# Kernel optimization log

Measured on AMD Instinct MI355X. Metric: run time of the kernel, lower is better.

## Reference

```python
import jax, jax.numpy as jnp
import numpy as np

N, C, H, W = 16, 512, 32, 32
OC = C // 8  # shrink = 8


def setup_inputs() -> dict:
    key = jax.random.key(0)
    ks = jax.random.split(key, 8)
    s = lambda fan: 1.0 / np.sqrt(fan)
    return {
        "tensor": jax.random.normal(ks[0], (N, C, H, W), dtype=jnp.float32),
        "key_w": jax.random.normal(ks[1], (OC, C), dtype=jnp.float32) * s(C),
        "key_b": jax.random.normal(ks[2], (OC,), dtype=jnp.float32) * 0.01,
        "query_w": jax.random.normal(ks[3], (OC, C), dtype=jnp.float32) * s(C),
        "query_b": jax.random.normal(ks[4], (OC,), dtype=jnp.float32) * 0.01,
        "value_w": jax.random.normal(ks[5], (C, C), dtype=jnp.float32) * s(C),
        "value_b": jax.random.normal(ks[6], (C,), dtype=jnp.float32) * 0.01,
        "gamma": jax.random.normal(ks[7], (1,), dtype=jnp.float32),
    }


def reference(tensor, key_w, key_b, query_w, query_b, value_w, value_b, gamma):
    n, c, h, w = tensor.shape
    x = tensor.reshape(n, c, h * w)  # [n, c, hw]
    # 1x1 convs are per-position linear maps over channels
    k = jnp.einsum("oc,ncp->nop", key_w, x) + key_b[None, :, None]      # [n, oc, hw]
    q = jnp.einsum("oc,ncp->nop", query_w, x) + query_b[None, :, None]  # [n, oc, hw]
    v = jnp.einsum("oc,ncp->nop", value_w, x) + value_b[None, :, None]  # [n, c, hw]
    # unscaled attention: softmax over keys (last dim)
    scores = jnp.einsum("ncq,nck->nqk", q, k)  # [n, hw, hw]
    attn = jax.nn.softmax(scores, axis=2)
    o = jnp.einsum("nck,nqk->ncq", v, attn).reshape(n, c, h, w)
    return tensor + o * gamma[0]
```

## Files before the change

kernel.cpp:

```cpp
#include <hip/hip_runtime.h>
#include <hip/hip_bf16.h>

typedef __hip_bfloat16 bf16;
typedef __attribute__((ext_vector_type(8))) short bf16x8;
typedef __attribute__((ext_vector_type(4))) float f32x4;

#define NBATCH 16
#define CCH    512
#define PP     1024
#define OCH    64

__device__ __forceinline__ void gload16(const void* g, void* l) {
  __builtin_amdgcn_global_load_lds(
      (const __attribute__((address_space(1))) void*)g,
      (__attribute__((address_space(3))) void*)l, 16, 0, 0);
}
__device__ __forceinline__ float bf2f(bf16 v) { return __bfloat162float(v); }
__device__ __forceinline__ bf16  f2bf(float v) { return __float2bfloat16(v); }

__device__ __forceinline__ void barrier_vm0() {
  asm volatile("s_waitcnt vmcnt(0)" ::: "memory");
  __builtin_amdgcn_s_barrier();
  asm volatile("" ::: "memory");
}
__device__ __forceinline__ void barrier_lgkm0() {
  asm volatile("s_waitcnt lgkmcnt(0)" ::: "memory");
  __builtin_amdgcn_s_barrier();
  asm volatile("" ::: "memory");
}

__global__ void prep_kernel(const float* __restrict__ key_w, const float* __restrict__ key_b,
                            const float* __restrict__ query_w, const float* __restrict__ query_b,
                            const float* __restrict__ value_w, const float* __restrict__ value_b,
                            bf16* __restrict__ wqk_hi, bf16* __restrict__ wqk_lo,
                            bf16* __restrict__ wv, float* __restrict__ bias_qk,
                            float* __restrict__ bias_v) {
  const int t = blockIdx.x * blockDim.x + threadIdx.x;
  const int TOT_QK = 128 * 512;
  const int TOT_V  = 512 * 512;
  if (t < TOT_QK) {
    const int m = t >> 9, c = t & 511;
    const float v = (m < 64) ? query_w[m * 512 + c] : key_w[(m - 64) * 512 + c];
    const bf16 hi = f2bf(v);
    wqk_hi[t] = hi;
    wqk_lo[t] = f2bf(v - bf2f(hi));
  } else if (t < TOT_QK + TOT_V) {
    const int u = t - TOT_QK;
    wv[u] = f2bf(value_w[u]);
  } else if (t < TOT_QK + TOT_V + 128) {
    const int m = t - (TOT_QK + TOT_V);
    bias_qk[m] = (m < 64) ? query_b[m] : key_b[m - 64];
  } else if (t < TOT_QK + TOT_V + 128 + 512) {
    const int m = t - (TOT_QK + TOT_V + 128);
    bias_v[m] = value_b[m];
  }
}

__global__ __launch_bounds__(256) void gemm_qkv_kernel(
    const bf16* __restrict__ Whi, const bf16* __restrict__ Wlo,
    const bf16* __restrict__ Wv, const float* __restrict__ x,
    const float* __restrict__ biasqk, const float* __restrict__ biasv,
    bf16* __restrict__ qhi, bf16* __restrict__ qlo,
    bf16* __restrict__ khi, bf16* __restrict__ klo,
    bf16* __restrict__ Vout) {
  __shared__ __align__(16) char sm[65536];
  const int tid = threadIdx.x, l = tid & 63, w = tid >> 6;
  const int li = l & 15, g = l >> 4;
  const int lrow = l >> 3, lcol = (l & 7) * 8, wr = w >> 1, wc = w & 1;
  const int tp = tid >> 1;
  const int tch = (tid & 1) * 32;
  const f32x4 z = {0.f, 0.f, 0.f, 0.f};
  f32x4 acc[4][4];
#pragma unroll
  for (int i = 0; i < 4; ++i)
#pragma unroll
    for (int j = 0; j < 4; ++j) acc[i][j] = z;

  char* Xs  = sm + 32768;
  char* Bsh = sm + 32768;
  char* Bsl = sm + 49152;

  if (blockIdx.x < 128) {
    const int id = blockIdx.x;
    const int n0 = (id & 7) * 128, bn = id >> 3;
    const float* xb = x + (size_t)bn * CCH * PP;
    bf16* Ash = (bf16*)sm;
    bf16* Asl = (bf16*)(sm + 16384);

    for (int kt = 0; kt < CCH; kt += 64) {
#pragma unroll
      for (int it = 0; it < 4; ++it) {
        const int chunk = w * 4 + it;
        const int ar = chunk * 8 + lrow;
        gload16(Whi + (size_t)ar * CCH + kt + lcol, &Ash[chunk * 512]);
        gload16(Wlo + (size_t)ar * CCH + kt + lcol, &Asl[chunk * 512]);
      }
#pragma unroll
      for (int i = 0; i < 8; ++i) {
        const int s = i * 256 + w * 64 + l;
        const int row = s >> 5, col16 = s & 31;
        gload16(xb + (size_t)(kt + row) * PP + n0 + col16 * 4,
                Xs + (i * 256 + w * 64) * 16);
      }
      __syncthreads();

      float f[32];
#pragma unroll
      for (int k = 0; k < 32; ++k)
        f[k] = *(const float*)(Xs + (size_t)(tch + k) * 512 + tp * 4);
      barrier_lgkm0();
#pragma unroll
      for (int k2 = 0; k2 < 4; ++k2) {
        bf16x8 hv, lv;
#pragma unroll
        for (int j = 0; j < 8; ++j) {
          const float ff = f[k2 * 8 + j];
          const bf16 h = f2bf(ff);
          const bf16 lo_ = f2bf(ff - bf2f(h));
          short hs, ls;
          __builtin_memcpy(&hs, &h, 2);
          __builtin_memcpy(&ls, &lo_, 2);
          hv[j] = hs;
          lv[j] = ls;
        }
        const int chunk = (tch >> 3) + k2;
        const int pu = chunk ^ (tp & 7);
        *(bf16x8*)(Bsh + tp * 128 + pu * 16) = hv;
        *(bf16x8*)(Bsl + tp * 128 + pu * 16) = lv;
      }
      barrier_lgkm0();

#pragma unroll
      for (int kk = 0; kk < 2; ++kk) {
        bf16x8 ah[4], al[4], bh[4], bl[4];
        const int ko = kk * 32 + g * 8;
#pragma unroll
        for (int i = 0; i < 4; ++i) {
          const int r = (wr * 64 + i * 16 + li) * 64 + ko;
          ah[i] = *(const bf16x8*)&Ash[r];
          al[i] = *(const bf16x8*)&Asl[r];
        }
#pragma unroll
        for (int j = 0; j < 4; ++j) {
          const int row = wc * 64 + j * 16 + li;
          const int pu = (4 * kk + g) ^ (row & 7);
          bh[j] = *(const bf16x8*)(Bsh + row * 128 + pu * 16);
          bl[j] = *(const bf16x8*)(Bsl + row * 128 + pu * 16);
        }
#pragma unroll
        for (int i = 0; i < 4; ++i)
#pragma unroll
          for (int j = 0; j < 4; ++j) {
            acc[i][j] = __builtin_amdgcn_mfma_f32_16x16x32_bf16(ah[i], bh[j], acc[i][j], 0, 0, 0);
            acc[i][j] = __builtin_amdgcn_mfma_f32_16x16x32_bf16(ah[i], bl[j], acc[i][j], 0, 0, 0);
            acc[i][j] = __builtin_amdgcn_mfma_f32_16x16x32_bf16(al[i], bh[j], acc[i][j], 0, 0, 0);
          }
      }
      __syncthreads();
    }
    const size_t qoff = (size_t)bn * PP * OCH;
#pragma unroll
    for (int i = 0; i < 4; ++i)
#pragma unroll
      for (int j = 0; j < 4; ++j)
#pragma unroll
        for (int r = 0; r < 4; ++r) {
          const int m = wr * 64 + i * 16 + g * 4 + r;
          const int p = n0 + wc * 64 + j * 16 + li;
          const float v = acc[i][j][r] + biasqk[m];
          const bf16 hi = f2bf(v);
          const bf16 lo = f2bf(v - bf2f(hi));
          if (m < 64) {
            qhi[qoff + (size_t)p * OCH + m] = hi;
            qlo[qoff + (size_t)p * OCH + m] = lo;
          } else {
            khi[qoff + (size_t)p * OCH + (m - 64)] = hi;
            klo[qoff + (size_t)p * OCH + (m - 64)] = lo;
          }
        }
  } else {
    const int id = blockIdx.x - 128;
    const int n0 = (id & 7) * 128, m0 = ((id >> 3) & 3) * 128, bn = id >> 5;
    const float* xb = x + (size_t)bn * CCH * PP;
    bf16* As = (bf16*)sm;

    for (int kt = 0; kt < CCH; kt += 64) {
#pragma unroll
      for (int it = 0; it < 4; ++it) {
        const int chunk = w * 4 + it;
        gload16(Wv + (size_t)(m0 + chunk * 8 + lrow) * CCH + kt + lcol, &As[chunk * 512]);
      }
#pragma unroll
      for (int i = 0; i < 8; ++i) {
        const int s = i * 256 + w * 64 + l;
        const int row = s >> 5, col16 = s & 31;
        gload16(xb + (size_t)(kt + row) * PP + n0 + col16 * 4,
                Xs + (i * 256 + w * 64) * 16);
      }
      __syncthreads();

      float f[32];
#pragma unroll
      for (int k = 0; k < 32; ++k)
        f[k] = *(const float*)(Xs + (size_t)(tch + k) * 512 + tp * 4);
      barrier_lgkm0();
#pragma unroll
      for (int k2 = 0; k2 < 4; ++k2) {
        bf16x8 hv;
#pragma unroll
        for (int j = 0; j < 8; ++j) {
          const bf16 h = f2bf(f[k2 * 8 + j]);
          short hs;
          __builtin_memcpy(&hs, &h, 2);
          hv[j] = hs;
        }
        const int chunk = (tch >> 3) + k2;
        const int pu = chunk ^ (tp & 7);
        *(bf16x8*)(Bsh + tp * 128 + pu * 16) = hv;
      }
      barrier_lgkm0();

#pragma unroll
      for (int kk = 0; kk < 2; ++kk) {
        bf16x8 a[4], b[4];
        const int ko = kk * 32 + g * 8;
#pragma unroll
        for (int i = 0; i < 4; ++i) a[i] = *(const bf16x8*)&As[(wr * 64 + i * 16 + li) * 64 + ko];
#pragma unroll
        for (int j = 0; j < 4; ++j) {
          const int row = wc * 64 + j * 16 + li;
          const int pu = (4 * kk + g) ^ (row & 7);
          b[j] = *(const bf16x8*)(Bsh + row * 128 + pu * 16);
        }
#pragma unroll
        for (int i = 0; i < 4; ++i)
#pragma unroll
          for (int j = 0; j < 4; ++j)
            acc[i][j] = __builtin_amdgcn_mfma_f32_16x16x32_bf16(a[i], b[j], acc[i][j], 0, 0, 0);
      }
      __syncthreads();
    }
#pragma unroll
    for (int i = 0; i < 4; ++i)
#pragma unroll
      for (int j = 0; j < 4; ++j)
#pragma unroll
        for (int r = 0; r < 4; ++r) {
          const int m = m0 + wr * 64 + i * 16 + g * 4 + r;
          const int p = n0 + wc * 64 + j * 16 + li;
          Vout[(size_t)bn * CCH * PP + (size_t)m * PP + p] = f2bf(acc[i][j][r] + biasv[m]);
        }
  }
}

#define KT 32
#define NT 32

__global__ __launch_bounds__(512, 2) void fused_attn_kernel(
    const bf16* __restrict__ qhi, const bf16* __restrict__ qlo,
    const bf16* __restrict__ khi, const bf16* __restrict__ klo,
    const bf16* __restrict__ vbuf, const float* __restrict__ tensor,
    const float* __restrict__ gamma, float* __restrict__ out) {
  __shared__ __align__(16) char smem[102400];
  __shared__ float red[128];
  __shared__ float fq[64];
  const int tid = threadIdx.x, l = tid & 63, w = tid >> 6;

  const int d = blockIdx.x;
  const int idx = d >> 3;
  const int bn = (d & 7) * 2 + (idx >> 4);
  const int qt0 = (idx & 15) * 64;

  const size_t qkoff = (size_t)bn * PP * OCH;
  const size_t voff  = (size_t)bn * CCH * PP;
  char* Qh = smem;
  char* Ql = smem + 8192;
  char* Pb = smem + 98304;

  {
    const int s = (w << 6) | l;
    const int row = s >> 3, pu = s & 7, lu = pu ^ (row & 7);
    const size_t src = qkoff + (size_t)(qt0 + row) * OCH + lu * 8;
    gload16(qhi + src, Qh + w * 1024);
    gload16(qlo + src, Ql + w * 1024);
  }
  barrier_vm0();

  bf16x8 ah[2], al[2];
  {
    const int qrow = ((w & 3) << 4) + (l & 15);
#pragma unroll
    for (int h = 0; h < 2; ++h) {
      const int lu = (l >> 4) + 4 * h, pu = lu ^ (qrow & 7);
      ah[h] = *(const bf16x8*)(Qh + qrow * 128 + pu * 16);
      al[h] = *(const bf16x8*)(Ql + qrow * 128 + pu * 16);
    }
  }

  auto stage_kv = [&](int t, char* khD, char* klD, char* vD) {
    {
      const int s = ((w & 3) << 6) | l;
      const int row = s >> 3, pu = s & 7, lu = pu ^ (row & 7);
      const bf16* srcp = ((w < 4) ? khi : klo) + qkoff + (size_t)(t * KT + row) * OCH + lu * 8;
      gload16(srcp, ((w < 4) ? khD : klD) + (w & 3) * 1024);
    }
#pragma unroll
    for (int c4 = 0; c4 < 4; ++c4) {
      const int s = (w << 8) + (c4 << 6) + l;
      const int row = s >> 2, pu = s & 3, lu = pu ^ ((row >> 1) & 3);
      const bf16* srcp = vbuf + voff + (size_t)row * PP + t * KT + lu * 8;
      gload16(srcp, vD + ((w << 8) + (c4 << 6)) * 16);
    }
  };

  stage_kv(0, smem + 16384, smem + 24576, smem + 32768);

  f32x4 acc[4][4];
  const f32x4 z = {0.f, 0.f, 0.f, 0.f};
#pragma unroll
  for (int i = 0; i < 4; ++i)
#pragma unroll
    for (int j = 0; j < 4; ++j) acc[i][j] = z;
  float psum[4] = {0.f, 0.f, 0.f, 0.f};
  const int kf = w >> 2;

  for (int t = 0; t < NT; ++t) {
    char* khB = smem + 16384 + ((t & 1) ? 4096 : 0);
    char* klB = smem + 24576 + ((t & 1) ? 4096 : 0);
    char* vB  = smem + 32768 + ((t & 1) ? 32768 : 0);

    barrier_vm0();

    if (t + 1 < NT) {
      stage_kv(t + 1,
               smem + 16384 + ((t & 1) ? 0 : 4096),
               smem + 24576 + ((t & 1) ? 0 : 4096),
               smem + 32768 + ((t & 1) ? 0 : 32768));
    }

    bf16x8 kh_[2], kl_[2];
    const int krow = (kf << 4) + (l & 15);
#pragma unroll
    for (int h = 0; h < 2; ++h) {
      const int lu = (l >> 4) + 4 * h, pu = lu ^ (krow & 7);
      kh_[h] = *(const bf16x8*)(khB + krow * 128 + pu * 16);
      kl_[h] = *(const bf16x8*)(klB + krow * 128 + pu * 16);
    }
    __builtin_amdgcn_s_setprio(1);
    f32x4 s = z;
    s = __builtin_amdgcn_mfma_f32_16x16x32_bf16(ah[0], kh_[0], s, 0, 0, 0);
    s = __builtin_amdgcn_mfma_f32_16x16x32_bf16(ah[1], kh_[1], s, 0, 0, 0);
    s = __builtin_amdgcn_mfma_f32_16x16x32_bf16(al[0], kh_[0], s, 0, 0, 0);
    s = __builtin_amdgcn_mfma_f32_16x16x32_bf16(al[1], kh_[1], s, 0, 0, 0);
    s = __builtin_amdgcn_mfma_f32_16x16x32_bf16(ah[0], kl_[0], s, 0, 0, 0);
    s = __builtin_amdgcn_mfma_f32_16x16x32_bf16(ah[1], kl_[1], s, 0, 0, 0);
    __builtin_amdgcn_s_setprio(0);

#pragma unroll
    for (int r = 0; r < 4; ++r) {
      const float pv = __expf(s[r] - 30.f);
      const bf16 pb16 = f2bf(pv);
      psum[r] += bf2f(pb16);
      const int q = ((w & 3) << 4) + ((l >> 4) << 2) + r;
      const int k = (kf << 4) + (l & 15);
      const int pu = (k >> 3) ^ ((q >> 1) & 3);
      *(bf16*)(Pb + q * 64 + pu * 16 + (k & 7) * 2) = pb16;
    }
    barrier_lgkm0();

    bf16x8 va[4], pb[4];
#pragma unroll
    for (int i = 0; i < 4; ++i) {
      const int crow = (w << 6) + (i << 4) + (l & 15);
      const int pu = (l >> 4) ^ ((crow >> 1) & 3);
      va[i] = *(const bf16x8*)(vB + crow * 64 + pu * 16);
    }
#pragma unroll
    for (int j = 0; j < 4; ++j) {
      const int prow = (j << 4) + (l & 15);
      const int pu = (l >> 4) ^ ((prow >> 1) & 3);
      pb[j] = *(const bf16x8*)(Pb + prow * 64 + pu * 16);
    }
    __builtin_amdgcn_s_setprio(1);
#pragma unroll
    for (int i = 0; i < 4; ++i)
#pragma unroll
      for (int j = 0; j < 4; ++j)
        acc[i][j] = __builtin_amdgcn_mfma_f32_16x16x32_bf16(va[i], pb[j], acc[i][j], 0, 0, 0);
    __builtin_amdgcn_s_setprio(0);
  }

  f32x4 tv0[8];
#pragma unroll
  for (int it = 0; it < 8; ++it) {
    const int chunk = it * 512 + tid;
    const int cl = chunk >> 4, ch = chunk & 15;
    tv0[it] = *(const f32x4*)&tensor[((size_t)bn * CCH + cl) * PP + qt0 + ch * 4];
  }

#pragma unroll
  for (int off = 1; off < 16; off <<= 1)
#pragma unroll
    for (int r = 0; r < 4; ++r) psum[r] += __shfl_xor(psum[r], off);
  if ((l & 15) == 0) {
#pragma unroll
    for (int r = 0; r < 4; ++r) {
      const int q = ((w & 3) << 4) + ((l >> 4) << 2) + r;
      red[q * 2 + kf] = psum[r];
    }
  }
  __syncthreads();
  if (tid < 64) fq[tid] = gamma[0] / (red[tid * 2] + red[tid * 2 + 1]);
  __syncthreads();

  float* rep = (float*)smem;
  for (int half = 0; half < 2; ++half) {
    if ((w >> 2) == half) {
#pragma unroll
      for (int i = 0; i < 4; ++i)
#pragma unroll
        for (int j = 0; j < 4; ++j) {
          const int q = (j << 4) + (l & 15);
          const float f = fq[q];
          const int c0 = ((w & 3) << 6) + (i << 4) + ((l >> 4) << 2);
#pragma unroll
          for (int r = 0; r < 4; ++r) rep[(c0 + r) * 68 + q] = acc[i][j][r] * f;
        }
    }
    __syncthreads();
#pragma unroll
    for (int it = 0; it < 8; ++it) {
      const int chunk = it * 512 + tid;
      const int cl = chunk >> 4, ch = chunk & 15;
      const size_t gi = ((size_t)bn * CCH + half * 256 + cl) * PP + qt0 + ch * 4;
      const f32x4 tv = (half == 0) ? tv0[it] : *(const f32x4*)&tensor[gi];
      const f32x4 rv = *(const f32x4*)&rep[cl * 68 + ch * 4];
      *(f32x4*)&out[gi] = tv + rv;
    }
    __syncthreads();
  }
}

extern "C" void kernel_launch(void* const* d_in, const int* in_sizes, int n_in,
                              void* d_out, int out_size, void* d_ws, size_t ws_size,
                              hipStream_t stream) {
  const float* tensor  = (const float*)d_in[0];
  const float* key_w   = (const float*)d_in[1];
  const float* key_b   = (const float*)d_in[2];
  const float* query_w = (const float*)d_in[3];
  const float* query_b = (const float*)d_in[4];
  const float* value_w = (const float*)d_in[5];
  const float* value_b = (const float*)d_in[6];
  const float* gamma   = (const float*)d_in[7];

  char* ws = (char*)d_ws;
  size_t off = 0;
  auto alloc = [&](size_t bytes) -> char* {
    char* p = ws + off;
    off += (bytes + 255) & ~(size_t)255;
    return p;
  };
  bf16* wqk_hi = (bf16*)alloc(128 * 512 * 2);
  bf16* wqk_lo = (bf16*)alloc(128 * 512 * 2);
  bf16* wv     = (bf16*)alloc(512 * 512 * 2);
  float* bias_qk = (float*)alloc(128 * 4);
  float* bias_v  = (float*)alloc(512 * 4);
  bf16* q_hi = (bf16*)alloc((size_t)NBATCH * PP * OCH * 2);
  bf16* q_lo = (bf16*)alloc((size_t)NBATCH * PP * OCH * 2);
  bf16* k_hi = (bf16*)alloc((size_t)NBATCH * PP * OCH * 2);
  bf16* k_lo = (bf16*)alloc((size_t)NBATCH * PP * OCH * 2);
  bf16* vbuf = (bf16*)alloc((size_t)NBATCH * CCH * PP * 2);
  (void)ws_size; (void)in_sizes; (void)n_in; (void)out_size;

  prep_kernel<<<dim3(1283), dim3(256), 0, stream>>>(
      key_w, key_b, query_w, query_b, value_w, value_b,
      wqk_hi, wqk_lo, wv, bias_qk, bias_v);

  gemm_qkv_kernel<<<dim3(640), dim3(256), 0, stream>>>(
      wqk_hi, wqk_lo, wv, tensor, bias_qk, bias_v,
      q_hi, q_lo, k_hi, k_lo, vbuf);

  fused_attn_kernel<<<dim3(256), dim3(512), 0, stream>>>(
      q_hi, q_lo, k_hi, k_lo, vbuf, tensor, gamma, (float*)d_out);
}
```

Measured before the change: 91.70 us.

## Prefetch next X tile during MFMA in projection GEMM loops

Restructures the QK and V projection loops so the next K-slice of the input tile is loaded into shared memory while the current slice's MFMAs run. B fragments are hoisted into registers before the prefetch so the aliased staging buffer can be overwritten safely. Partial vmcnt waits replace full syncs so weight loads stay in flight. Register pressure rises from holding both k-halves of B fragments.

```diff
diff --git a/kernel.cpp b/kernel.cpp
--- a/kernel.cpp
+++ b/kernel.cpp
@@ -87,6 +87,17 @@
     bf16* Ash = (bf16*)sm;
     bf16* Asl = (bf16*)(sm + 16384);
 
+    auto stage_x = [&](int kt) {
+#pragma unroll
+      for (int i = 0; i < 8; ++i) {
+        const int s = i * 256 + w * 64 + l;
+        const int row = s >> 5, col16 = s & 31;
+        gload16(xb + (size_t)(kt + row) * PP + n0 + col16 * 4,
+                Xs + (i * 256 + w * 64) * 16);
+      }
+    };
+    stage_x(0);
+
     for (int kt = 0; kt < CCH; kt += 64) {
 #pragma unroll
       for (int it = 0; it < 4; ++it) {
@@ -95,20 +106,18 @@
         gload16(Whi + (size_t)ar * CCH + kt + lcol, &Ash[chunk * 512]);
         gload16(Wlo + (size_t)ar * CCH + kt + lcol, &Asl[chunk * 512]);
       }
-#pragma unroll
-      for (int i = 0; i < 8; ++i) {
-        const int s = i * 256 + w * 64 + l;
-        const int row = s >> 5, col16 = s & 31;
-        gload16(xb + (size_t)(kt + row) * PP + n0 + col16 * 4,
-                Xs + (i * 256 + w * 64) * 16);
-      }
-      __syncthreads();
+      asm volatile("s_waitcnt vmcnt(8)" ::: "memory");
+      __builtin_amdgcn_s_barrier();
+      asm volatile("" ::: "memory");
 
       float f[32];
 #pragma unroll
       for (int k = 0; k < 32; ++k)
         f[k] = *(const float*)(Xs + (size_t)(tch + k) * 512 + tp * 4);
-      barrier_lgkm0();
+      asm volatile("s_waitcnt vmcnt(0) lgkmcnt(0)" ::: "memory");
+      __builtin_amdgcn_s_barrier();
+      asm volatile("" ::: "memory");
+
 #pragma unroll
       for (int k2 = 0; k2 < 4; ++k2) {
         bf16x8 hv, lv;
@@ -130,9 +139,23 @@
       }
       barrier_lgkm0();
 
+      bf16x8 bh[2][4], bl[2][4];
+#pragma unroll
+      for (int kk = 0; kk < 2; ++kk)
+#pragma unroll
+        for (int j = 0; j < 4; ++j) {
+          const int row = wc * 64 + j * 16 + li;
+          const int pu = (4 * kk + g) ^ (row & 7);
+          bh[kk][j] = *(const bf16x8*)(Bsh + row * 128 + pu * 16);
+          bl[kk][j] = *(const bf16x8*)(Bsl + row * 128 + pu * 16);
+        }
+      barrier_lgkm0();
+
+      if (kt + 64 < CCH) stage_x(kt + 64);
+
 #pragma unroll
       for (int kk = 0; kk < 2; ++kk) {
-        bf16x8 ah[4], al[4], bh[4], bl[4];
+        bf16x8 ah[4], al[4];
         const int ko = kk * 32 + g * 8;
 #pragma unroll
         for (int i = 0; i < 4; ++i) {
@@ -141,22 +164,17 @@
           al[i] = *(const bf16x8*)&Asl[r];
         }
 #pragma unroll
-        for (int j = 0; j < 4; ++j) {
-          const int row = wc * 64 + j * 16 + li;
-          const int pu = (4 * kk + g) ^ (row & 7);
-          bh[j] = *(const bf16x8*)(Bsh + row * 128 + pu * 16);
-          bl[j] = *(const bf16x8*)(Bsl + row * 128 + pu * 16);
-        }
-#pragma unroll
         for (int i = 0; i < 4; ++i)
 #pragma unroll
           for (int j = 0; j < 4; ++j) {
-            acc[i][j] = __builtin_amdgcn_mfma_f32_16x16x32_bf16(ah[i], bh[j], acc[i][j], 0, 0, 0);
-            acc[i][j] = __builtin_amdgcn_mfma_f32_16x16x32_bf16(ah[i], bl[j], acc[i][j], 0, 0, 0);
-            acc[i][j] = __builtin_amdgcn_mfma_f32_16x16x32_bf16(al[i], bh[j], acc[i][j], 0, 0, 0);
+            acc[i][j] = __builtin_amdgcn_mfma_f32_16x16x32_bf16(ah[i], bh[kk][j], acc[i][j], 0, 0, 0);
+            acc[i][j] = __builtin_amdgcn_mfma_f32_16x16x32_bf16(ah[i], bl[kk][j], acc[i][j], 0, 0, 0);
+            acc[i][j] = __builtin_amdgcn_mfma_f32_16x16x32_bf16(al[i], bh[kk][j], acc[i][j], 0, 0, 0);
           }
       }
-      __syncthreads();
+      asm volatile("" ::: "memory");
+      __builtin_amdgcn_s_barrier();
+      asm volatile("" ::: "memory");
     }
     const size_t qoff = (size_t)bn * PP * OCH;
 #pragma unroll
@@ -184,12 +202,7 @@
     const float* xb = x + (size_t)bn * CCH * PP;
     bf16* As = (bf16*)sm;
 
-    for (int kt = 0; kt < CCH; kt += 64) {
-#pragma unroll
-      for (int it = 0; it < 4; ++it) {
-        const int chunk = w * 4 + it;
-        gload16(Wv + (size_t)(m0 + chunk * 8 + lrow) * CCH + kt + lcol, &As[chunk * 512]);
-      }
+    auto stage_x = [&](int kt) {
 #pragma unroll
       for (int i = 0; i < 8; ++i) {
         const int s = i * 256 + w * 64 + l;
@@ -197,13 +210,27 @@
         gload16(xb + (size_t)(kt + row) * PP + n0 + col16 * 4,
                 Xs + (i * 256 + w * 64) * 16);
       }
-      __syncthreads();
+    };
+    stage_x(0);
+
+    for (int kt = 0; kt < CCH; kt += 64) {
+#pragma unroll
+      for (int it = 0; it < 4; ++it) {
+        const int chunk = w * 4 + it;
+        gload16(Wv + (size_t)(m0 + chunk * 8 + lrow) * CCH + kt + lcol, &As[chunk * 512]);
+      }
+      asm volatile("s_waitcnt vmcnt(4)" ::: "memory");
+      __builtin_amdgcn_s_barrier();
+      asm volatile("" ::: "memory");
 
       float f[32];
 #pragma unroll
       for (int k = 0; k < 32; ++k)
         f[k] = *(const float*)(Xs + (size_t)(tch + k) * 512 + tp * 4);
-      barrier_lgkm0();
+      asm volatile("s_waitcnt vmcnt(0) lgkmcnt(0)" ::: "memory");
+      __builtin_amdgcn_s_barrier();
+      asm volatile("" ::: "memory");
+
 #pragma unroll
       for (int k2 = 0; k2 < 4; ++k2) {
         bf16x8 hv;
@@ -220,25 +247,35 @@
       }
       barrier_lgkm0();
 
-#pragma unroll
-      for (int kk = 0; kk < 2; ++kk) {
-        bf16x8 a[4], b[4];
-        const int ko = kk * 32 + g * 8;
-#pragma unroll
-        for (int i = 0; i < 4; ++i) a[i] = *(const bf16x8*)&As[(wr * 64 + i * 16 + li) * 64 + ko];
+      bf16x8 b[2][4];
+#pragma unroll
+      for (int kk = 0; kk < 2; ++kk)
 #pragma unroll
         for (int j = 0; j < 4; ++j) {
           const int row = wc * 64 + j * 16 + li;
           const int pu = (4 * kk + g) ^ (row & 7);
-          b[j] = *(const bf16x8*)(Bsh + row * 128 + pu * 16);
-        }
+          b[kk][j] = *(const bf16x8*)(Bsh + row * 128 + pu * 16);
+        }
+      barrier_lgkm0();
+
+      if (kt + 64 < CCH) stage_x(kt + 64);
+
+#pragma unroll
+      for (int kk = 0; kk < 2; ++kk) {
+        bf16x8 a[4];
+        const int ko = kk * 32 + g * 8;
 #pragma unroll
         for (int i = 0; i < 4; ++i)
+          a[i] = *(const bf16x8*)&As[(wr * 64 + i * 16 + li) * 64 + ko];
+#pragma unroll
+        for (int i = 0; i < 4; ++i)
 #pragma unroll
           for (int j = 0; j < 4; ++j)
-            acc[i][j] = __builtin_amdgcn_mfma_f32_16x16x32_bf16(a[i], b[j], acc[i][j], 0, 0, 0);
-      }
-      __syncthreads();
+            acc[i][j] = __builtin_amdgcn_mfma_f32_16x16x32_bf16(a[i], b[kk][j], acc[i][j], 0, 0, 0);
+      }
+      asm volatile("" ::: "memory");
+      __builtin_amdgcn_s_barrier();
+      asm volatile("" ::: "memory");
     }
 #pragma unroll
     for (int i = 0; i < 4; ++i)
```

After: 88.32 us. 1.04x faster.
